# Performance work log

Hardware: AMD Instinct MI355X
Metric: run time of the kernel (lower is better)

The kernel has to match this reference:

```python
import jax, jax.numpy as jnp
import numpy as np

B, S, D, H = 4, 1024, 1024, 16
HD = D // H
MAX_DIST, WIN, MAX_SPAN = 512, 256, 512
TEMP_SCALE = 0.01
EPS = 1e-5


def _ln(x, g, b):
    m = x.mean(-1, keepdims=True)
    v = ((x - m) ** 2).mean(-1, keepdims=True)
    return (x - m) * jax.lax.rsqrt(v + EPS) * g + b


def _heads(t):
    b, s, _ = t.shape
    return t.reshape(b, s, H, HD).transpose(0, 2, 1, 3)


def _merge(t):
    b, _, s, _ = t.shape
    return t.transpose(0, 2, 1, 3).reshape(b, s, D)


def _global_attn(x, Wq, bq, Wk, Wv, bv, Wo, bo):
    # MultiheadC with mask tensor passed -> is_causal=True SDPA (default 1/sqrt(HD) scale)
    q = _heads(x @ Wq.T + bq)
    k = _heads(x @ Wk.T)
    v = _heads(x @ Wv.T + bv)
    s = jnp.einsum('bhqd,bhkd->bhqk', q, k) / float(np.sqrt(HD))
    n = x.shape[1]
    causal = jnp.tril(jnp.ones((n, n), bool))
    s = jnp.where(causal, s, jnp.finfo(s.dtype).min)
    w = jax.nn.softmax(s, axis=-1)
    return _merge(jnp.einsum('bhqk,bhkd->bhqd', w, v)) @ Wo.T + bo


def _span_attn(q, k, v, temp):
    # AdaptiveSpan core: softmax(QK^T / temperature * head_dim**-0.25) V
    scale = HD ** -0.25
    qh, kh, vh = _heads(q), _heads(k), _heads(v)
    w = jax.nn.softmax(jnp.einsum('bhqd,bhkd->bhqk', qh, kh) / temp * scale, axis=-1)
    return _merge(jnp.einsum('bhqk,bhkd->bhqd', w, vh))


def _slide_win(local, span_mean, win, span_len, local_max):
    bx, sx, dx = local.shape
    temp = 1.0 + TEMP_SCALE * (1.0 - span_mean)  # sharpen=True branch
    outs = []
    for st in range(0, sx, win):  # static unrolled loop over windows (ragged slices)
        en = min(st + win, sx)
        wlen = en - st
        ks = max(0, st - span_len + win)
        ke = min(st + span_len, sx)
        klen = ke - ks
        eff = min(int(wlen * span_mean), wlen, klen, local_max)
        if eff <= 0:
            outs.append(jnp.zeros((bx, wlen, dx), local.dtype))
            continue
        o = _span_attn(local[:, st:st + eff], local[:, ks:ks + eff], local[:, ks:ks + eff], temp)
        if eff < wlen:
            o = jnp.concatenate([o, jnp.zeros((bx, wlen - eff, dx), local.dtype)], axis=1)
        outs.append(o)
    return jnp.concatenate(outs, axis=1)


def setup_inputs() -> dict:
    key = jax.random.key(0)
    ks = jax.random.split(key, 8)
    qkv_std = 1.0 / float(np.sqrt(HD))
    return {
        'x': jax.random.normal(ks[0], (B, S, D), jnp.float32),
        'ln_a_g': jnp.ones((D,), jnp.float32),
        'ln_a_b': jnp.zeros((D,), jnp.float32),
        'ln_b_g': jnp.ones((D,), jnp.float32),
        'ln_b_b': jnp.zeros((D,), jnp.float32),
        'Wq': jax.random.normal(ks[1], (D, D), jnp.float32) * qkv_std,
        'bq': jnp.zeros((D,), jnp.float32),
        'Wk': jax.random.normal(ks[2], (D, D), jnp.float32) * qkv_std,
        'Wv': jax.random.normal(ks[3], (D, D), jnp.float32) * qkv_std,
        'bv': jnp.zeros((D,), jnp.float32),
        'Wo': jax.random.normal(ks[4], (D, D), jnp.float32) * 0.02,
        'bo': jnp.zeros((D,), jnp.float32),
        'Wp': jax.random.normal(ks[5], (1, D), jnp.float32) * float(np.sqrt(2.0 / (D + 1))),
        'bp': jnp.zeros((1,), jnp.float32),
        'Wproj': jax.random.normal(ks[6], (D, 2 * D), jnp.float32) * 0.02,
        'bproj': jnp.zeros((D,), jnp.float32),
    }


def reference(x, ln_a_g, ln_a_b, ln_b_g, ln_b_b, Wq, bq, Wk, Wv, bv, Wo, bo, Wp, bp, Wproj, bproj):
    local = _ln(x, ln_a_g, ln_a_b)
    globe = _ln(x, ln_b_g, ln_b_b)
    globe_out = _global_attn(globe, Wq, bq, Wk, Wv, bv, Wo, bo)
    # Predictor: sigmoid(Linear(mean over seq))
    base_scale = jax.nn.sigmoid(globe_out.mean(axis=1) @ Wp.T + bp)  # [B, 1]
    span_scale = jnp.clip(base_scale, 0.0, 1.0)  # RL refine factor fixed at 1.0 (deterministic)
    span_mean = float(jnp.mean(span_scale))  # mirrors torch .item() host sync
    win = max(1, int(WIN * span_mean))
    span_len = max(1, int(MAX_SPAN * span_mean))
    local_max = min(MAX_DIST, span_len, win)
    local_out = _slide_win(local, span_mean, win, span_len, local_max)
    combined = jnp.concatenate([local_out, globe_out], axis=-1)
    return combined @ Wproj.T + bproj
```

## Files before the change

kernel.cpp:

```cpp
#include <hip/hip_runtime.h>
#include <math.h>

#define B_ 4
#define S_ 1024
#define D_ 1024
#define H_ 16
#define HD_ 64
#define BSD_ (B_*S_*D_)

using short8 = __attribute__((ext_vector_type(8))) short;
using f32x4  = __attribute__((ext_vector_type(4))) float;

#define MFMA16(a,b,c) __builtin_amdgcn_mfma_f32_16x16x32_bf16((a),(b),(c),0,0,0)

__device__ __forceinline__ ushort f2bf(float f) {
  uint u = __float_as_uint(f);
  return (ushort)((u + 0x7fffu + ((u >> 16) & 1u)) >> 16);
}
__device__ __forceinline__ float bf2f(ushort h) {
  return __uint_as_float(((uint)h) << 16);
}
__device__ __forceinline__ void split8(const float* p, short8* hi, short8* lo) {
  #pragma unroll
  for (int j = 0; j < 8; j++) {
    ushort h = f2bf(p[j]);
    (*hi)[j] = (short)h;
    (*lo)[j] = (short)f2bf(p[j] - bf2f(h));
  }
}
__device__ __forceinline__ void async_load16(const ushort* g, ushort* l) {
  __builtin_amdgcn_global_load_lds(
      (const __attribute__((address_space(1))) unsigned int*)g,
      (__attribute__((address_space(3))) unsigned int*)l, 16, 0, 0);
}

__device__ __forceinline__ float block_reduce_sum_256(float v, float* sbuf) {
  #pragma unroll
  for (int off = 32; off > 0; off >>= 1) v += __shfl_xor(v, off, 64);
  int lane = threadIdx.x & 63, wid = threadIdx.x >> 6;
  __syncthreads();
  if (lane == 0) sbuf[wid] = v;
  __syncthreads();
  return sbuf[0] + sbuf[1] + sbuf[2] + sbuf[3];
}

__device__ __forceinline__ void split4_store(const float4 a, ushort* orow, int c, int stride) {
  ushort4 hi, lo;
  hi.x = f2bf(a.x); hi.y = f2bf(a.y); hi.z = f2bf(a.z); hi.w = f2bf(a.w);
  lo.x = f2bf(a.x - bf2f(hi.x)); lo.y = f2bf(a.y - bf2f(hi.y));
  lo.z = f2bf(a.z - bf2f(hi.z)); lo.w = f2bf(a.w - bf2f(hi.w));
  *(ushort4*)(orow + c)          = hi;
  *(ushort4*)(orow + stride + c) = lo;
}

__global__ __launch_bounds__(256) void prep_kernel(
    const float* __restrict__ x,
    const float* __restrict__ ln_a_g, const float* __restrict__ ln_a_b,
    const float* __restrict__ ln_b_g, const float* __restrict__ ln_b_b,
    const float* __restrict__ Wq, const float* __restrict__ Wk,
    const float* __restrict__ Wv, const float* __restrict__ bq,
    const float* __restrict__ bv, const float* __restrict__ Wo,
    const float* __restrict__ Wproj,
    ushort* __restrict__ Acat, ushort* __restrict__ Bqkv,
    float* __restrict__ biascat, float* __restrict__ loc,
    ushort* __restrict__ B3, ushort* __restrict__ Bo) {
  __shared__ float sbuf[4];
  const int bx = blockIdx.x;
  const int t = threadIdx.x;
  if (bx < 4096) {
    const int row = bx;
    const int c = t*4;
    const float* xr = x + (size_t)row * D_;
    float4 v = *(const float4*)(xr + c);
    float s = v.x + v.y + v.z + v.w;
    const float mean = block_reduce_sum_256(s, sbuf) * (1.0f/D_);
    float4 dv = make_float4(v.x-mean, v.y-mean, v.z-mean, v.w-mean);
    float sq = dv.x*dv.x + dv.y*dv.y + dv.z*dv.z + dv.w*dv.w;
    const float var = block_reduce_sum_256(sq, sbuf) * (1.0f/D_);
    const float r = rsqrtf(var + 1e-5f);
    float4 gg = *(const float4*)(ln_b_g + c);
    float4 bb = *(const float4*)(ln_b_b + c);
    float4 n;
    n.x = dv.x*r*gg.x + bb.x; n.y = dv.y*r*gg.y + bb.y;
    n.z = dv.z*r*gg.z + bb.z; n.w = dv.w*r*gg.w + bb.w;
    split4_store(n, Acat + (size_t)row*2048, c, 1024);
  } else if (bx < 7168) {
    const int idx = (bx - 4096)*256 + t;
    const int n = idx >> 8;
    const int col4 = (idx & 255) << 2;
    const float* src = (n < 1024) ? (Wq + (size_t)n*1024)
                     : (n < 2048) ? (Wk + (size_t)(n-1024)*1024)
                                  : (Wv + (size_t)(n-2048)*1024);
    const float4 a = *(const float4*)(src + col4);
    split4_store(a, Bqkv + (size_t)n*2048, col4, 1024);
    if (idx < 3072)
      biascat[idx] = (idx < 1024) ? bq[idx] : (idx < 2048) ? 0.f : bv[idx-2048];
  } else if (bx < 11264) {
    const int row = bx - 7168;
    const float* xr = x + (size_t)row * D_;
    float v[4]; float s = 0.f;
    #pragma unroll
    for (int i = 0; i < 4; i++) { v[i] = xr[t + 256*i]; s += v[i]; }
    const float mean = block_reduce_sum_256(s, sbuf) * (1.0f/D_);
    float sq = 0.f;
    #pragma unroll
    for (int i = 0; i < 4; i++) { float d = v[i]-mean; sq += d*d; }
    const float var = block_reduce_sum_256(sq, sbuf) * (1.0f/D_);
    const float r = rsqrtf(var + 1e-5f);
    float* orow = loc + (size_t)row * D_;
    #pragma unroll
    for (int i = 0; i < 4; i++) {
      int c = t + 256*i;
      orow[c] = (v[i]-mean)*r*ln_a_g[c] + ln_a_b[c];
    }
  } else if (bx < 13312) {
    const int idx = (bx - 11264)*256 + t;
    const int row = idx >> 9;
    const int col4 = (idx & 511) << 2;
    const float4 a = *(const float4*)(Wproj + (size_t)row*2048 + col4);
    ushort4 hi;
    hi.x = f2bf(a.x); hi.y = f2bf(a.y); hi.z = f2bf(a.z); hi.w = f2bf(a.w);
    *(ushort4*)(B3 + (size_t)row*2048 + col4) = hi;
  } else {
    const int idx = (bx - 13312)*256 + t;
    const int n = idx >> 8;
    const int col4 = (idx & 255) << 2;
    const float4 a = *(const float4*)(Wo + (size_t)n*1024 + col4);
    split4_store(a, Bo + (size_t)n*2048, col4, 1024);
  }
}

__global__ __launch_bounds__(256) void mfma_gemm_qkv(
    const ushort* __restrict__ A, const ushort* __restrict__ Bw,
    const float* __restrict__ bias,
    ushort* __restrict__ Qsp, ushort* __restrict__ Ksp,
    ushort* __restrict__ Vth, ushort* __restrict__ Vtl, int Kh) {
  __shared__ __align__(16) ushort smem[17408];
  ushort* Ash = smem;
  ushort* Asl = smem + 4096;
  ushort* Bsh = smem + 8192;
  ushort* Bsl = smem + 12288;
  const int lda = 2*Kh;
  const int tid = threadIdx.x;
  const int bm = blockIdx.y * 128, bn = blockIdx.x * 128;
  const int wave = tid >> 6, lane = tid & 63;
  const int wm = wave >> 1, wn = wave & 1;
  const int lm = lane & 15, q = lane >> 4;
  const int lrow = lane >> 2;
  const int sw = (((lane & 3) ^ ((lane >> 3) & 3)) << 3);

  f32x4 acc[4][4];
  #pragma unroll
  for (int i = 0; i < 4; i++)
    #pragma unroll
    for (int j = 0; j < 4; j++)
      acc[i][j] = (f32x4){0.f,0.f,0.f,0.f};

  const ushort* Agh = A  + (size_t)(bm + wave*32 + lrow)*lda + sw;
  const ushort* Agl = Agh + Kh;
  const ushort* Bgh = Bw + (size_t)(bn + wave*32 + lrow)*lda + sw;
  const ushort* Bgl = Bgh + Kh;
  const size_t r16a = (size_t)16*lda;
  ushort* AhD0 = &Ash[(wave*32)*32];      ushort* AhD1 = &Ash[(wave*32+16)*32];
  ushort* AlD0 = &Asl[(wave*32)*32];      ushort* AlD1 = &Asl[(wave*32+16)*32];
  ushort* BhD0 = &Bsh[(wave*32)*32];      ushort* BhD1 = &Bsh[(wave*32+16)*32];
  ushort* BlD0 = &Bsl[(wave*32)*32];      ushort* BlD1 = &Bsl[(wave*32+16)*32];
  const int rsw  = ((q ^ ((lm >> 1) & 3)) << 3);
  const int aoff = (wm*64 + lm)*32 + rsw;
  const int boff = (wn*64 + lm)*32 + rsw;

  for (int k0 = 0; k0 < Kh; k0 += 32) {
    __syncthreads();
    async_load16(Agh + k0, AhD0);
    async_load16(Agh + r16a + k0, AhD1);
    async_load16(Agl + k0, AlD0);
    async_load16(Agl + r16a + k0, AlD1);
    async_load16(Bgh + k0, BhD0);
    async_load16(Bgh + r16a + k0, BhD1);
    async_load16(Bgl + k0, BlD0);
    async_load16(Bgl + r16a + k0, BlD1);
    __syncthreads();
    short8 ah[4], al[4], bh[4], bl[4];
    #pragma unroll
    for (int mt = 0; mt < 4; mt++) {
      ah[mt] = *(const short8*)&Ash[aoff + mt*512];
      al[mt] = *(const short8*)&Asl[aoff + mt*512];
    }
    #pragma unroll
    for (int nt = 0; nt < 4; nt++) {
      bh[nt] = *(const short8*)&Bsh[boff + nt*512];
      bl[nt] = *(const short8*)&Bsl[boff + nt*512];
    }
    #pragma unroll
    for (int mt = 0; mt < 4; mt++)
      #pragma unroll
      for (int nt = 0; nt < 4; nt++) {
        f32x4 a = acc[mt][nt];
        a = MFMA16(ah[mt], bh[nt], a);
        a = MFMA16(al[mt], bh[nt], a);
        a = MFMA16(ah[mt], bl[nt], a);
        acc[mt][nt] = a;
      }
  }

  const int b = bm >> 10, s0 = bm & 1023;
  if (blockIdx.x < 16) {
    ushort* dst = (blockIdx.x < 8) ? Qsp : Ksp;
    const int h = ((bn + wn*64) >> 6) & 15;
    #pragma unroll
    for (int mt = 0; mt < 4; mt++) {
      #pragma unroll
      for (int nt = 0; nt < 4; nt++) {
        const int n = bn + wn*64 + nt*16 + lm;
        const int d = nt*16 + lm;
        const float bb = bias[n];
        #pragma unroll
        for (int reg = 0; reg < 4; reg++) {
          const int s = s0 + wm*64 + mt*16 + q*4 + reg;
          const float val = acc[mt][nt][reg] + bb;
          const ushort hi = f2bf(val);
          const ushort lo = f2bf(val - bf2f(hi));
          ushort* rp = dst + ((size_t)((b*16 + h)*1024 + s))*128;
          rp[d] = hi; rp[64 + d] = lo;
        }
      }
    }
  } else {
    ushort* Th = smem;
    ushort* Tl = smem + 8704;
    #pragma unroll
    for (int c = 0; c < 2; c++) {
      __syncthreads();
      if (wn == c) {
        #pragma unroll
        for (int mt = 0; mt < 4; mt++)
          #pragma unroll
          for (int nt = 0; nt < 4; nt++) {
            const int nl = nt*16 + lm;
            const float bb = bias[bn + c*64 + nl];
            #pragma unroll
            for (int reg = 0; reg < 4; reg++) {
              const int sl = wm*64 + mt*16 + q*4 + reg;
              const float val = acc[mt][nt][reg] + bb;
              const ushort hi = f2bf(val);
              const ushort lo = f2bf(val - bf2f(hi));
              Th[nl*136 + sl] = hi;
              Tl[nl*136 + sl] = lo;
            }
          }
      }
      __syncthreads();
      const int nl = tid >> 2, s32 = (tid & 3)*32;
      const int h = ((bn - 2048 + c*64) >> 6) & 15;
      const size_t drow = ((size_t)((b*16 + h)*64 + nl))*1024 + s0 + s32;
      #pragma unroll
      for (int j = 0; j < 4; j++) {
        *(short8*)(Vth + drow + j*8) = *(const short8*)&Th[nl*136 + s32 + j*8];
        *(short8*)(Vtl + drow + j*8) = *(const short8*)&Tl[nl*136 + s32 + j*8];
      }
    }
  }
}

__global__ __launch_bounds__(256) void mfma_gemm2(
    const ushort* __restrict__ A, const ushort* __restrict__ Bw,
    const float* __restrict__ bias, float* __restrict__ C,
    int Kh, int ldc, ushort* __restrict__ aux) {
  __shared__ __align__(16) ushort Ash[64*32];
  __shared__ __align__(16) ushort Asl[64*32];
  __shared__ __align__(16) ushort Bsh[128*32];
  __shared__ __align__(16) ushort Bsl[128*32];
  const int lda = 2*Kh;
  const int tid = threadIdx.x;
  const int bm = blockIdx.y * 64, bn = blockIdx.x * 128;
  const int wave = tid >> 6, lane = tid & 63;
  const int lm = lane & 15, q = lane >> 4;
  const int lrow = lane >> 2;
  const int sw = (((lane & 3) ^ ((lane >> 3) & 3)) << 3);

  f32x4 acc[4][2];
  #pragma unroll
  for (int i = 0; i < 4; i++)
    #pragma unroll
    for (int j = 0; j < 2; j++)
      acc[i][j] = (f32x4){0.f,0.f,0.f,0.f};

  const ushort* gsrc[6];
  ushort* ldst[6];
  #pragma unroll
  for (int i = 0; i < 6; i++) {
    const int s = wave*6 + i;
    const ushort* gp; ushort* lp;
    if (s < 4)       { gp = A  + (size_t)(bm + s*16 + lrow)*lda + sw;           lp = &Ash[(s*16)*32]; }
    else if (s < 8)  { gp = A  + (size_t)(bm + (s-4)*16 + lrow)*lda + Kh + sw;  lp = &Asl[((s-4)*16)*32]; }
    else if (s < 16) { gp = Bw + (size_t)(bn + (s-8)*16 + lrow)*lda + sw;       lp = &Bsh[((s-8)*16)*32]; }
    else             { gp = Bw + (size_t)(bn + (s-16)*16 + lrow)*lda + Kh + sw; lp = &Bsl[((s-16)*16)*32]; }
    gsrc[i] = gp; ldst[i] = lp;
  }
  const int rsw = ((q ^ ((lm >> 1) & 3)) << 3);
  const int aoff = lm*32 + rsw;
  const int boff = (wave*32 + lm)*32 + rsw;

  for (int k0 = 0; k0 < Kh; k0 += 32) {
    __syncthreads();
    #pragma unroll
    for (int i = 0; i < 6; i++) async_load16(gsrc[i] + k0, ldst[i]);
    __syncthreads();
    short8 ah[4], al[4], bh[2], bl[2];
    #pragma unroll
    for (int mt = 0; mt < 4; mt++) {
      ah[mt] = *(const short8*)&Ash[aoff + mt*512];
      al[mt] = *(const short8*)&Asl[aoff + mt*512];
    }
    #pragma unroll
    for (int nt = 0; nt < 2; nt++) {
      bh[nt] = *(const short8*)&Bsh[boff + nt*512];
      bl[nt] = *(const short8*)&Bsl[boff + nt*512];
    }
    #pragma unroll
    for (int mt = 0; mt < 4; mt++)
      #pragma unroll
      for (int nt = 0; nt < 2; nt++) {
        f32x4 a = acc[mt][nt];
        a = MFMA16(ah[mt], bh[nt], a);
        a = MFMA16(al[mt], bh[nt], a);
        a = MFMA16(ah[mt], bl[nt], a);
        acc[mt][nt] = a;
      }
  }

  #pragma unroll
  for (int mt = 0; mt < 4; mt++) {
    #pragma unroll
    for (int nt = 0; nt < 2; nt++) {
      const int n = bn + wave*32 + nt*16 + lm;
      const float bb = bias ? bias[n] : 0.f;
      #pragma unroll
      for (int reg = 0; reg < 4; reg++) {
        const int m = bm + mt*16 + q*4 + reg;
        const float val = acc[mt][nt][reg] + bb;
        C[(size_t)m*ldc + n] = val;
        if (aux) aux[(size_t)m*2048 + 1024 + n] = f2bf(val);
      }
    }
  }
}

__global__ __launch_bounds__(256) void mfma_gemm(
    const ushort* __restrict__ A, const ushort* __restrict__ Bw,
    const float* __restrict__ bias, float* __restrict__ C,
    int K, int ldc) {
  __shared__ __align__(16) ushort As[64*32];
  __shared__ __align__(16) ushort Bs[128*32];
  const int tid = threadIdx.x;
  const int bm = blockIdx.y * 64, bn = blockIdx.x * 128;
  const int wave = tid >> 6, lane = tid & 63;
  const int lm = lane & 15, q = lane >> 4;
  const int lrow = lane >> 2;
  const int sw = (((lane & 3) ^ ((lane >> 3) & 3)) << 3);

  f32x4 acc[4][2];
  #pragma unroll
  for (int i = 0; i < 4; i++)
    #pragma unroll
    for (int j = 0; j < 2; j++)
      acc[i][j] = (f32x4){0.f,0.f,0.f,0.f};

  const ushort* gsrc[3];
  ushort* ldst[3];
  #pragma unroll
  for (int i = 0; i < 3; i++) {
    const int s = wave*3 + i;
    const ushort* gp; ushort* lp;
    if (s < 4) { gp = A  + (size_t)(bm + s*16 + lrow)*K + sw;     lp = &As[(s*16)*32]; }
    else       { gp = Bw + (size_t)(bn + (s-4)*16 + lrow)*K + sw; lp = &Bs[((s-4)*16)*32]; }
    gsrc[i] = gp; ldst[i] = lp;
  }
  const int rsw = ((q ^ ((lm >> 1) & 3)) << 3);
  const int aoff = lm*32 + rsw;
  const int boff = (wave*32 + lm)*32 + rsw;

  for (int k0 = 0; k0 < K; k0 += 32) {
    __syncthreads();
    #pragma unroll
    for (int i = 0; i < 3; i++) async_load16(gsrc[i] + k0, ldst[i]);
    __syncthreads();
    short8 af[4], bf[2];
    #pragma unroll
    for (int mt = 0; mt < 4; mt++) af[mt] = *(const short8*)&As[aoff + mt*512];
    #pragma unroll
    for (int nt = 0; nt < 2; nt++) bf[nt] = *(const short8*)&Bs[boff + nt*512];
    #pragma unroll
    for (int mt = 0; mt < 4; mt++)
      #pragma unroll
      for (int nt = 0; nt < 2; nt++)
        acc[mt][nt] = MFMA16(af[mt], bf[nt], acc[mt][nt]);
  }

  #pragma unroll
  for (int mt = 0; mt < 4; mt++) {
    #pragma unroll
    for (int nt = 0; nt < 2; nt++) {
      const int n = bn + wave*32 + nt*16 + lm;
      const float bb = bias ? bias[n] : 0.f;
      #pragma unroll
      for (int reg = 0; reg < 4; reg++) {
        const int m = bm + mt*16 + q*4 + reg;
        C[(size_t)m*ldc + n] = acc[mt][nt][reg] + bb;
      }
    }
  }
}

__device__ __forceinline__ void attn_unit(
    int qt, int kt, int w, int lm, int q,
    const short8 qh[2], const short8 ql[2],
    const ushort* Kc, const ushort* Vc, float* Pf,
    f32x4 of[4], float mst[4], float lst[4]) {
  f32x4 sS[4];
  #pragma unroll
  for (int nt = 0; nt < 4; nt++) {
    const ushort* kr = &Kc[(nt*16 + lm)*136 + q*8];
    const short8 kh0 = *(const short8*)(kr);
    const short8 kh1 = *(const short8*)(kr + 32);
    const short8 kl0 = *(const short8*)(kr + 64);
    const short8 kl1 = *(const short8*)(kr + 96);
    f32x4 a = (f32x4){0.f,0.f,0.f,0.f};
    a = MFMA16(qh[0], kh0, a);
    a = MFMA16(ql[0], kh0, a);
    a = MFMA16(qh[0], kl0, a);
    a = MFMA16(qh[1], kh1, a);
    a = MFMA16(ql[1], kh1, a);
    a = MFMA16(qh[1], kl1, a);
    sS[nt] = a;
  }
  const int ktbase = kt*64;
  const int qrow0 = qt*64 + w*16 + q*4;
  #pragma unroll
  for (int rm = 0; rm < 4; rm++) {
    const int qrow = qrow0 + rm;
    float v[4];
    #pragma unroll
    for (int nt = 0; nt < 4; nt++) {
      const int kcol = ktbase + nt*16 + lm;
      const float x = sS[nt][rm]*0.125f;
      v[nt] = (kcol <= qrow) ? x : -INFINITY;
    }
    float tm = fmaxf(fmaxf(v[0],v[1]), fmaxf(v[2],v[3]));
    #pragma unroll
    for (int off = 1; off < 16; off <<= 1) tm = fmaxf(tm, __shfl_xor(tm, off, 64));
    const float nm = fmaxf(mst[rm], tm);
    const float alpha = __expf(mst[rm] - nm);
    float ps = 0.f;
    #pragma unroll
    for (int nt = 0; nt < 4; nt++) {
      float p = __expf(v[nt] - nm);
      sS[nt][rm] = p;
      ps += p;
    }
    #pragma unroll
    for (int off = 1; off < 16; off <<= 1) ps += __shfl_xor(ps, off, 64);
    lst[rm] = lst[rm]*alpha + ps;
    mst[rm] = nm;
    #pragma unroll
    for (int nt = 0; nt < 4; nt++) of[nt][rm] *= alpha;
  }
  #pragma unroll
  for (int rm = 0; rm < 4; rm++)
    #pragma unroll
    for (int nt = 0; nt < 4; nt++)
      Pf[(w*16 + q*4 + rm)*66 + nt*16 + lm] = sS[nt][rm];
  short8 ph[2], pl[2];
  {
    const float* prow = &Pf[(w*16 + lm)*66];
    float pv[16];
    *(float4*)&pv[0]  = *(const float4*)(prow + q*8);
    *(float4*)&pv[4]  = *(const float4*)(prow + q*8 + 4);
    *(float4*)&pv[8]  = *(const float4*)(prow + 32 + q*8);
    *(float4*)&pv[12] = *(const float4*)(prow + 32 + q*8 + 4);
    split8(&pv[0], &ph[0], &pl[0]);
    split8(&pv[8], &ph[1], &pl[1]);
  }
  #pragma unroll
  for (int nt = 0; nt < 4; nt++) {
    const ushort* vr = &Vc[(nt*16 + lm)*136 + q*8];
    const short8 vh0 = *(const short8*)(vr);
    const short8 vh1 = *(const short8*)(vr + 32);
    const short8 vl0 = *(const short8*)(vr + 64);
    const short8 vl1 = *(const short8*)(vr + 96);
    f32x4 a = of[nt];
    a = MFMA16(ph[0], vh0, a);
    a = MFMA16(pl[0], vh0, a);
    a = MFMA16(ph[0], vl0, a);
    a = MFMA16(ph[1], vh1, a);
    a = MFMA16(pl[1], vh1, a);
    a = MFMA16(ph[1], vl1, a);
    of[nt] = a;
  }
}

__global__ __launch_bounds__(256) void gattn_mfma(
    const ushort* __restrict__ Qsp, const ushort* __restrict__ Ksp,
    const ushort* __restrict__ Vth, const ushort* __restrict__ Vtl,
    ushort* __restrict__ Aout) {
  __shared__ __align__(16) ushort Kc[64*136];
  __shared__ __align__(16) ushort Vc[64*136];
  __shared__ __align__(16) float  Pf[64*66];
  const int bh = blockIdx.y;
  const int b = bh >> 4, h = bh & 15;
  const int tid = threadIdx.x;
  const int w = tid >> 6, lane = tid & 63;
  const int lm = lane & 15, q = lane >> 4;
  const ushort* Qb_ = Qsp + (size_t)bh * (1024*128);
  const ushort* Kb_ = Ksp + (size_t)bh * (1024*128);
  const ushort* Vhb = Vth + (size_t)bh * (64*1024);
  const ushort* Vlb = Vtl + (size_t)bh * (64*1024);
  const int qtA = 15 - blockIdx.x;
  const int qtB = blockIdx.x;

  short8 qhA[2], qlA[2], qhB[2], qlB[2];
  {
    const ushort* qr = Qb_ + (size_t)(qtA*64 + w*16 + lm)*128 + q*8;
    qhA[0] = *(const short8*)(qr);
    qhA[1] = *(const short8*)(qr + 32);
    qlA[0] = *(const short8*)(qr + 64);
    qlA[1] = *(const short8*)(qr + 96);
    const ushort* qr2 = Qb_ + (size_t)(qtB*64 + w*16 + lm)*128 + q*8;
    qhB[0] = *(const short8*)(qr2);
    qhB[1] = *(const short8*)(qr2 + 32);
    qlB[0] = *(const short8*)(qr2 + 64);
    qlB[1] = *(const short8*)(qr2 + 96);
  }
  f32x4 ofA[4], ofB[4];
  float mstA[4], lstA[4], mstB[4], lstB[4];
  #pragma unroll
  for (int nt = 0; nt < 4; nt++) {
    ofA[nt] = (f32x4){0.f,0.f,0.f,0.f};
    ofB[nt] = (f32x4){0.f,0.f,0.f,0.f};
  }
  #pragma unroll
  for (int rm = 0; rm < 4; rm++) {
    mstA[rm] = -INFINITY; lstA[rm] = 0.f;
    mstB[rm] = -INFINITY; lstB[rm] = 0.f;
  }

  for (int kt = 0; kt <= qtA; ++kt) {
    __syncthreads();
    #pragma unroll
    for (int i = 0; i < 4; i++) {
      const int slot = i*256 + tid;
      const int row = slot >> 4, c8 = slot & 15;
      *(float4*)&Kc[row*136 + c8*8] =
          *(const float4*)(Kb_ + (size_t)(kt*64 + row)*128 + c8*8);
      const ushort* vsrc = ((c8 < 8) ? Vhb : Vlb) + (size_t)row*1024 + kt*64 + (c8&7)*8;
      *(float4*)&Vc[row*136 + c8*8] = *(const float4*)vsrc;
    }
    __syncthreads();
    attn_unit(qtA, kt, w, lm, q, qhA, qlA, Kc, Vc, Pf, ofA, mstA, lstA);
    if (kt <= qtB)
      attn_unit(qtB, kt, w, lm, q, qhB, qlB, Kc, Vc, Pf, ofB, mstB, lstB);
  }

  #pragma unroll
  for (int rm = 0; rm < 4; rm++) {
    const float invA = 1.0f / lstA[rm];
    const int sA = qtA*64 + w*16 + q*4 + rm;
    ushort* arow = Aout + ((size_t)(b*1024 + sA))*2048 + h*64;
    #pragma unroll
    for (int nt = 0; nt < 4; nt++) {
      const float val = ofA[nt][rm] * invA;
      const ushort hi = f2bf(val);
      arow[nt*16 + lm] = hi;
      arow[1024 + nt*16 + lm] = f2bf(val - bf2f(hi));
    }
    const float invB = 1.0f / lstB[rm];
    const int sB = qtB*64 + w*16 + q*4 + rm;
    ushort* brow = Aout + ((size_t)(b*1024 + sB))*2048 + h*64;
    #pragma unroll
    for (int nt = 0; nt < 4; nt++) {
      const float val = ofB[nt][rm] * invB;
      const ushort hi = f2bf(val);
      brow[nt*16 + lm] = hi;
      brow[1024 + nt*16 + lm] = f2bf(val - bf2f(hi));
    }
  }
}

__global__ __launch_bounds__(256) void seqmean1_kernel(const float* __restrict__ g,
                                                       float* __restrict__ part) {
  const int d = blockIdx.x*256 + threadIdx.x;
  const int sc = blockIdx.y;
  const int b = blockIdx.z;
  const float* p = g + ((size_t)b*S_ + sc*128)*D_ + d;
  float s = 0.f;
  #pragma unroll 4
  for (int i = 0; i < 128; i++) s += p[(size_t)i*D_];
  part[((size_t)(b*8 + sc))*D_ + d] = s;
}
__global__ __launch_bounds__(256) void seqmean2_kernel(const float* __restrict__ part,
                                                       float* __restrict__ mbd) {
  const int d = blockIdx.x*256 + threadIdx.x;
  const int b = blockIdx.y;
  float s = 0.f;
  #pragma unroll
  for (int i = 0; i < 8; i++) s += part[((size_t)(b*8 + i))*D_ + d];
  mbd[b*D_ + d] = s * (1.0f/S_);
}

__global__ __launch_bounds__(256) void predictor_kernel(
    const float* __restrict__ mbd, const float* __restrict__ Wp,
    const float* __restrict__ bp, float* __restrict__ fpar, int* __restrict__ ipar) {
  __shared__ float sbuf[4];
  __shared__ float sdots[4];
  const int tid = threadIdx.x;
  for (int b = 0; b < 4; b++) {
    float psum = 0.f;
    for (int d = tid; d < D_; d += 256) psum += mbd[b*D_ + d]*Wp[d];
    float tot = block_reduce_sum_256(psum, sbuf);
    if (tid == 0) sdots[b] = tot;
  }
  __syncthreads();
  if (tid == 0) {
    float smv = 0.f;
    for (int b = 0; b < 4; b++) {
      float z = sdots[b] + bp[0];
      smv += 1.0f/(1.0f + expf(-z));
    }
    smv *= 0.25f;
    int win = max(1, (int)(256.0f*smv));
    int span_len = max(1, (int)(512.0f*smv));
    int local_max = min(512, min(span_len, win));
    float temp = 1.0f + 0.01f*(1.0f - smv);
    int n_win = (S_ + win - 1)/win;
    fpar[0] = smv; fpar[1] = temp;
    ipar[0] = win; ipar[1] = span_len; ipar[2] = local_max; ipar[3] = n_win;
  }
}

#define LDP 68
__global__ __launch_bounds__(256) void lattn_kernel(
    const float* __restrict__ Lc, ushort* __restrict__ Out,
    const int* __restrict__ ip, const float* __restrict__ fpp) {
  __shared__ __align__(16) float Qs[HD_][LDP];
  __shared__ __align__(16) float KPs[64][LDP];
  __shared__ __align__(16) float Vs[64][LDP];
  const int n_win = ip[3];
  const int win = ip[0], span_len = ip[1], local_max = ip[2];
  const float sm = fpp[0], temp = fpp[1];
  const int bh = blockIdx.y;
  const int b = bh >> 4, h = bh & 15;
  const int tid = threadIdx.x;
  const int tx = tid & 15, ty = tid >> 4;
  const float sc = 0.35355339059327373f / temp;
  for (int w = blockIdx.x; w < n_win; w += gridDim.x) {
    const int st = w * win;
    const int en = min(st + win, S_); const int wlen = en - st;
    const int ks = max(0, st - span_len + win);
    const int ke = min(st + span_len, S_); const int klen = ke - ks;
    int eff = (int)((double)wlen * (double)sm);
    eff = min(min(eff, wlen), min(klen, local_max));
    if (eff > 0) {
      const int nt = (eff + 63) >> 6;
      for (int qt = 0; qt < nt; ++qt) {
        const int qn = min(64, eff - qt*64);
        __syncthreads();
        #pragma unroll
        for (int c = 0; c < 4; c++) {
          int f = tid + c*256;
          int r = f >> 4;
          int dc = (f & 15) << 2;
          float4 q4 = make_float4(0.f,0.f,0.f,0.f);
          if (r < qn) q4 = *(const float4*)(Lc + ((size_t)(b*S_ + st + qt*64 + r)) * D_ + h*HD_ + dc);
          Qs[dc+0][r]=q4.x; Qs[dc+1][r]=q4.y; Qs[dc+2][r]=q4.z; Qs[dc+3][r]=q4.w;
        }
        float o[4][4] = {{0.f,0.f,0.f,0.f},{0.f,0.f,0.f,0.f},{0.f,0.f,0.f,0.f},{0.f,0.f,0.f,0.f}};
        float mrow[4], lrow[4];
        #pragma unroll
        for (int i=0;i<4;i++){ mrow[i] = -INFINITY; lrow[i] = 0.f; }
        for (int kt = 0; kt < nt; ++kt) {
          const int kn = min(64, eff - kt*64);
          __syncthreads();
          #pragma unroll
          for (int c = 0; c < 4; c++) {
            int f = tid + c*256;
            int r = f >> 4;
            int dc = (f & 15) << 2;
            float4 k4 = make_float4(0.f,0.f,0.f,0.f);
            if (r < kn) k4 = *(const float4*)(Lc + ((size_t)(b*S_ + ks + kt*64 + r)) * D_ + h*HD_ + dc);
            KPs[dc+0][r]=k4.x; KPs[dc+1][r]=k4.y; KPs[dc+2][r]=k4.z; KPs[dc+3][r]=k4.w;
            *(float4*)&Vs[r][dc] = k4;
          }
          __syncthreads();
          float s[4][4] = {{0.f,0.f,0.f,0.f},{0.f,0.f,0.f,0.f},{0.f,0.f,0.f,0.f},{0.f,0.f,0.f,0.f}};
          #pragma unroll 8
          for (int d = 0; d < HD_; ++d) {
            const float4 a  = *(const float4*)&Qs[d][ty*4];
            const float4 bb = *(const float4*)&KPs[d][tx*4];
            const float av[4]={a.x,a.y,a.z,a.w};
            const float bv[4]={bb.x,bb.y,bb.z,bb.w};
            #pragma unroll
            for (int i=0;i<4;i++)
              #pragma unroll
              for (int j=0;j<4;j++)
                s[i][j] += av[i]*bv[j];
          }
          #pragma unroll
          for (int i=0;i<4;i++) {
            #pragma unroll
            for (int j=0;j<4;j++) {
              float lg = s[i][j]*sc;
              if (kt*64 + tx*4 + j >= eff) lg = -INFINITY;
              s[i][j] = lg;
            }
          }
          #pragma unroll
          for (int i=0;i<4;i++) {
            float tm = fmaxf(fmaxf(s[i][0],s[i][1]), fmaxf(s[i][2],s[i][3]));
            #pragma unroll
            for (int off=1; off<16; off<<=1) tm = fmaxf(tm, __shfl_xor(tm, off, 64));
            const float nm = fmaxf(mrow[i], tm);
            const float alpha = __expf(mrow[i]-nm);
            float ps = 0.f;
            #pragma unroll
            for (int j=0;j<4;j++){ float p = __expf(s[i][j]-nm); s[i][j]=p; ps += p; }
            #pragma unroll
            for (int off=1; off<16; off<<=1) ps += __shfl_xor(ps, off, 64);
            lrow[i] = lrow[i]*alpha + ps;
            mrow[i] = nm;
            #pragma unroll
            for (int j=0;j<4;j++) o[i][j] *= alpha;
          }
          __syncthreads();
          #pragma unroll
          for (int i=0;i<4;i++)
            #pragma unroll
            for (int j=0;j<4;j++)
              KPs[tx*4+j][ty*4+i] = s[i][j];
          __syncthreads();
          #pragma unroll 8
          for (int kk = 0; kk < 64; ++kk) {
            const float4 a  = *(const float4*)&KPs[kk][ty*4];
            const float4 bb = *(const float4*)&Vs[kk][tx*4];
            const float av[4]={a.x,a.y,a.z,a.w};
            const float bv[4]={bb.x,bb.y,bb.z,bb.w};
            #pragma unroll
            for (int i=0;i<4;i++)
              #pragma unroll
              for (int j=0;j<4;j++)
                o[i][j] += av[i]*bv[j];
          }
        }
        #pragma unroll
        for (int i=0;i<4;i++){
          const int r = ty*4 + i;
          if (r < qn) {
            const float inv = 1.0f / lrow[i];
            ushort4 ov;
            ov.x = f2bf(o[i][0]*inv); ov.y = f2bf(o[i][1]*inv);
            ov.z = f2bf(o[i][2]*inv); ov.w = f2bf(o[i][3]*inv);
            *(ushort4*)(Out + ((size_t)(b*S_ + st + qt*64 + r)) * 2048 + h*HD_ + tx*4) = ov;
          }
        }
      }
    }
    const ushort4 z = {0,0,0,0};
    for (int r = max(eff, 0) + ty; r < wlen; r += 16)
      *(ushort4*)(Out + ((size_t)(b*S_ + st + r)) * 2048 + h*HD_ + tx*4) = z;
  }
}

extern "C" void kernel_launch(void* const* d_in, const int* in_sizes, int n_in,
                              void* d_out, int out_size, void* d_ws, size_t ws_size,
                              hipStream_t stream) {
  const float* x      = (const float*)d_in[0];
  const float* ln_a_g = (const float*)d_in[1];
  const float* ln_a_b = (const float*)d_in[2];
  const float* ln_b_g = (const float*)d_in[3];
  const float* ln_b_b = (const float*)d_in[4];
  const float* Wq     = (const float*)d_in[5];
  const float* bq     = (const float*)d_in[6];
  const float* Wk     = (const float*)d_in[7];
  const float* Wv     = (const float*)d_in[8];
  const float* bv     = (const float*)d_in[9];
  const float* Wo     = (const float*)d_in[10];
  const float* bo     = (const float*)d_in[11];
  const float* Wp     = (const float*)d_in[12];
  const float* bp     = (const float*)d_in[13];
  const float* Wproj  = (const float*)d_in[14];
  const float* bproj  = (const float*)d_in[15];
  float* out = (float*)d_out;
  float* ws  = (float*)d_ws;
  ushort* wsu = (ushort*)d_ws;

  ushort* Qsp = wsu;
  ushort* Ksp = wsu + 8388608;
  ushort* Vth = wsu + 16777216;
  ushort* Vtl = wsu + 20971520;
  ushort* B3  = (ushort*)(ws + 12582912);
  float* glo  = ws + 16777216;
  float* loc  = ws + 20971520;
  float* biascat = ws + 25165824;
  float* mbd  = biascat + 4096;
  float* fpar = mbd + 4096;
  int*   ipar = (int*)(fpar + 8);
  ushort* Acat  = (ushort*)(ws + 25182208);
  ushort* Bqkv  = Acat + 12582912;
  ushort* Bo    = Bqkv + 9437184;
  float*  part = (float*)Acat;
  ushort* A3  = wsu;

  const dim3 blk(256);

  prep_kernel<<<dim3(14336), blk, 0, stream>>>(
      x, ln_a_g, ln_a_b, ln_b_g, ln_b_b, Wq, Wk, Wv, bq, bv, Wo, Wproj,
      Acat, Bqkv, biascat, loc, B3, Bo);
  mfma_gemm_qkv<<<dim3(24, 32), blk, 0, stream>>>(Acat, Bqkv, biascat,
                                                  Qsp, Ksp, Vth, Vtl, 1024);
  gattn_mfma<<<dim3(8, 64), blk, 0, stream>>>(Qsp, Ksp, Vth, Vtl, Acat);
  mfma_gemm2<<<dim3(8, 64), blk, 0, stream>>>(Acat, Bo, bo, glo, 1024, 1024, A3);
  seqmean1_kernel<<<dim3(4, 8, B_), blk, 0, stream>>>(glo, part);
  seqmean2_kernel<<<dim3(4, B_), blk, 0, stream>>>(part, mbd);
  predictor_kernel<<<dim3(1), blk, 0, stream>>>(mbd, Wp, bp, fpar, ipar);
  lattn_kernel<<<dim3(64, B_*H_), blk, 0, stream>>>(loc, A3, ipar, fpar);
  mfma_gemm<<<dim3(8, 64), blk, 0, stream>>>(A3, B3, bproj, out, 2048, 1024);
}
```

Baseline: 447.1 us.

## Add 256x256 eight-wave QKV GEMM with double-buffered async LDS pipeline

Replaces the 128x128 four-wave QKV projection GEMM with a 256x256-tile, 512-thread kernel. It uses 128KB of dynamic LDS double buffering, async global-to-LDS loads interleaved with MFMA phases, explicit vmcnt waits and barriers, setprio around compute, and a grid swizzle across 192 blocks. The aim is more operand reuse and better overlap of loads with split-bf16 MFMA work. In exchange it brings heavy register pressure, a grid of only 192 blocks (tail and occupancy risk), and a fallback path if the large LDS attribute fails.

```diff
diff --git a/kernel.cpp b/kernel.cpp
--- a/kernel.cpp
+++ b/kernel.cpp
@@ -130,6 +130,179 @@
   }
 }
 
+#define BARRIER() asm volatile("s_barrier" ::: "memory")
+#define VMW4 asm volatile("s_waitcnt vmcnt(4)" ::: "memory")
+#define VMW0 asm volatile("s_waitcnt vmcnt(0)" ::: "memory")
+
+#define STAGE_A(half, k0, SBs) do { \
+  _Pragma("unroll") \
+  for (int i_ = 0; i_ < 2; ++i_) { \
+    const int cid_ = wave*2 + i_; \
+    const int hilo_ = cid_ >> 3; const int seg_ = cid_ & 7; \
+    const int row0_ = (seg_>>2)*128 + (seg_&3)*16 + (half)*64; \
+    async_load16(A + ((size_t)(bm + row0_ + lrow) << 11) + (hilo_ << 10) + (k0) + sw, \
+                 (SBs) + hilo_*8192 + row0_*32); \
+  } } while (0)
+
+#define STAGE_B(half, k0, SBs) do { \
+  _Pragma("unroll") \
+  for (int i_ = 0; i_ < 2; ++i_) { \
+    const int cid_ = wave*2 + i_; \
+    const int hilo_ = cid_ >> 3; const int seg_ = cid_ & 7; \
+    const int row0_ = (seg_>>1)*64 + (seg_&1)*16 + (half)*32; \
+    async_load16(Bw + ((size_t)(bn + row0_ + lrow) << 11) + (hilo_ << 10) + (k0) + sw, \
+                 (SBs) + 16384 + hilo_*8192 + row0_*32); \
+  } } while (0)
+
+#define PH(mh, nh, SBc, STG, WT) do { \
+  short8 ah_[4], al_[4], bh_[2], bl_[2]; \
+  _Pragma("unroll") \
+  for (int m4_ = 0; m4_ < 4; ++m4_) { \
+    const int ro_ = (wm*128 + (mh)*64 + m4_*16 + lm)*32 + rsw; \
+    ah_[m4_] = *(const short8*)&(SBc)[ro_]; \
+    al_[m4_] = *(const short8*)&(SBc)[8192 + ro_]; } \
+  _Pragma("unroll") \
+  for (int n2_ = 0; n2_ < 2; ++n2_) { \
+    const int ro_ = (wn*64 + (nh)*32 + n2_*16 + lm)*32 + rsw; \
+    bh_[n2_] = *(const short8*)&(SBc)[16384 + ro_]; \
+    bl_[n2_] = *(const short8*)&(SBc)[24576 + ro_]; } \
+  STG; \
+  WT; \
+  BARRIER(); \
+  __builtin_amdgcn_s_setprio(1); \
+  _Pragma("unroll") \
+  for (int m4_ = 0; m4_ < 4; ++m4_) \
+    _Pragma("unroll") \
+    for (int n2_ = 0; n2_ < 2; ++n2_) { \
+      f32x4 t_ = acc[(mh)*4+m4_][(nh)*2+n2_]; \
+      t_ = MFMA16(ah_[m4_], bh_[n2_], t_); \
+      t_ = MFMA16(al_[m4_], bh_[n2_], t_); \
+      t_ = MFMA16(ah_[m4_], bl_[n2_], t_); \
+      acc[(mh)*4+m4_][(nh)*2+n2_] = t_; } \
+  __builtin_amdgcn_s_setprio(0); \
+  BARRIER(); \
+} while (0)
+
+#define GROUP(t, SBc, SBs) do { \
+  const int k0n_ = (((t) + 1) & 31) * 32; \
+  PH(0, 0, (SBc), STAGE_A(0, k0n_, (SBs)), VMW4); \
+  PH(0, 1, (SBc), STAGE_B(0, k0n_, (SBs)), VMW4); \
+  PH(1, 0, (SBc), STAGE_B(1, k0n_, (SBs)), ((void)0)); \
+  PH(1, 1, (SBc), STAGE_A(1, k0n_, (SBs)), VMW4); \
+} while (0)
+
+__global__ __launch_bounds__(512, 2) void qkv8_kernel(
+    const ushort* __restrict__ A, const ushort* __restrict__ Bw,
+    const float* __restrict__ bias,
+    ushort* __restrict__ Qsp, ushort* __restrict__ Ksp,
+    ushort* __restrict__ Vth, ushort* __restrict__ Vtl) {
+  extern __shared__ __align__(16) ushort smem[];
+  const int tid = threadIdx.x;
+  const int wave = tid >> 6, lane = tid & 63;
+  const int wm = wave >> 2, wn = wave & 3;
+  const int lm = lane & 15, q = lane >> 4;
+  const int lrow = lane >> 2;
+  const int sw = (((lane & 3) ^ ((lane >> 3) & 3)) << 3);
+  const int rsw = ((q ^ ((lm >> 1) & 3)) << 3);
+  const int bid = blockIdx.x;
+  const int swz = (bid & 7) * 24 + (bid >> 3);
+  const int bm = (swz / 12) * 256;
+  const int bn = (swz % 12) * 256;
+
+  f32x4 acc[8][4];
+  #pragma unroll
+  for (int i = 0; i < 8; ++i)
+    #pragma unroll
+    for (int j = 0; j < 4; ++j) acc[i][j] = (f32x4){0.f,0.f,0.f,0.f};
+
+  STAGE_A(0, 0, smem); STAGE_B(0, 0, smem); STAGE_B(1, 0, smem); STAGE_A(1, 0, smem);
+  VMW0; BARRIER();
+
+  #pragma unroll 1
+  for (int g = 0; g < 32; g += 2) {
+    GROUP(g,     smem,         smem + 32768);
+    GROUP(g + 1, smem + 32768, smem);
+  }
+  VMW0;
+  __syncthreads();
+
+  const int b = bm >> 10, s0 = bm & 1023;
+  if (bn < 2048) {
+    ushort* dst = (bn < 1024) ? Qsp : Ksp;
+    #pragma unroll
+    for (int m = 0; m < 8; ++m) {
+      const int s = s0 + wm*128 + m*16 + q*4;
+      #pragma unroll
+      for (int n = 0; n < 4; ++n) {
+        const int ncol = bn + wn*64 + n*16 + lm;
+        const int h = (ncol >> 6) & 15;
+        const int d = ncol & 63;
+        const float bb = bias[ncol];
+        #pragma unroll
+        for (int reg = 0; reg < 4; ++reg) {
+          const float val = acc[m][n][reg] + bb;
+          const ushort hi = f2bf(val);
+          ushort* rp = dst + ((size_t)((b*16 + h)*1024 + (s + reg)))*128;
+          rp[d] = hi; rp[64 + d] = f2bf(val - bf2f(hi));
+        }
+      }
+    }
+  } else {
+    const int h = ((bn - 2048) >> 6) + wn;
+    ushort* Tbuf = smem + wn * 8704;
+    const size_t vrow0 = (size_t)((b*16 + h) * 64);
+    #pragma unroll 1
+    for (int r = 0; r < 2; ++r) {
+      __syncthreads();
+      if (wm == r) {
+        #pragma unroll
+        for (int m = 0; m < 8; ++m)
+          #pragma unroll
+          for (int n = 0; n < 4; ++n) {
+            const int d = n*16 + lm;
+            const float bb = bias[bn + wn*64 + d];
+            #pragma unroll
+            for (int reg = 0; reg < 4; ++reg)
+              Tbuf[d*136 + m*16 + q*4 + reg] = f2bf(acc[m][n][reg] + bb);
+          }
+        #pragma unroll
+        for (int dd = 0; dd < 4; ++dd) {
+          const int d = (lane >> 2) + dd*16;
+          #pragma unroll
+          for (int j = 0; j < 4; ++j) {
+            const int sc = (lane & 3)*32 + j*8;
+            *(short8*)(Vth + (vrow0 + d)*1024 + s0 + wm*128 + sc) =
+                *(const short8*)&Tbuf[d*136 + sc];
+          }
+        }
+        #pragma unroll
+        for (int m = 0; m < 8; ++m)
+          #pragma unroll
+          for (int n = 0; n < 4; ++n) {
+            const int d = n*16 + lm;
+            const float bb = bias[bn + wn*64 + d];
+            #pragma unroll
+            for (int reg = 0; reg < 4; ++reg) {
+              const float val = acc[m][n][reg] + bb;
+              const ushort hi = f2bf(val);
+              Tbuf[d*136 + m*16 + q*4 + reg] = f2bf(val - bf2f(hi));
+            }
+          }
+        #pragma unroll
+        for (int dd = 0; dd < 4; ++dd) {
+          const int d = (lane >> 2) + dd*16;
+          #pragma unroll
+          for (int j = 0; j < 4; ++j) {
+            const int sc = (lane & 3)*32 + j*8;
+            *(short8*)(Vtl + (vrow0 + d)*1024 + s0 + wm*128 + sc) =
+                *(const short8*)&Tbuf[d*136 + sc];
+          }
+        }
+      }
+    }
+  }
+}
+
 __global__ __launch_bounds__(256) void mfma_gemm_qkv(
     const ushort* __restrict__ A, const ushort* __restrict__ Bw,
     const float* __restrict__ bias,
@@ -206,12 +379,12 @@
   const int b = bm >> 10, s0 = bm & 1023;
   if (blockIdx.x < 16) {
     ushort* dst = (blockIdx.x < 8) ? Qsp : Ksp;
-    const int h = ((bn + wn*64) >> 6) & 15;
     #pragma unroll
     for (int mt = 0; mt < 4; mt++) {
       #pragma unroll
       for (int nt = 0; nt < 4; nt++) {
         const int n = bn + wn*64 + nt*16 + lm;
+        const int h = (n >> 6) & 15;
         const int d = nt*16 + lm;
         const float bb = bias[n];
         #pragma unroll
@@ -811,11 +984,23 @@
 
   const dim3 blk(256);
 
+  static int qkv_path = -1;
+  if (qkv_path < 0) {
+    hipError_t e = hipFuncSetAttribute(
+        reinterpret_cast<const void*>(qkv8_kernel),
+        hipFuncAttributeMaxDynamicSharedMemorySize, 131072);
+    qkv_path = (e == hipSuccess) ? 1 : 0;
+  }
+
   prep_kernel<<<dim3(14336), blk, 0, stream>>>(
       x, ln_a_g, ln_a_b, ln_b_g, ln_b_b, Wq, Wk, Wv, bq, bv, Wo, Wproj,
       Acat, Bqkv, biascat, loc, B3, Bo);
-  mfma_gemm_qkv<<<dim3(24, 32), blk, 0, stream>>>(Acat, Bqkv, biascat,
-                                                  Qsp, Ksp, Vth, Vtl, 1024);
+  if (qkv_path)
+    qkv8_kernel<<<dim3(192), dim3(512), 131072, stream>>>(
+        Acat, Bqkv, biascat, Qsp, Ksp, Vth, Vtl);
+  else
+    mfma_gemm_qkv<<<dim3(24, 32), blk, 0, stream>>>(Acat, Bqkv, biascat,
+                                                    Qsp, Ksp, Vth, Vtl, 1024);
   gattn_mfma<<<dim3(8, 64), blk, 0, stream>>>(Qsp, Ksp, Vth, Vtl, Acat);
   mfma_gemm2<<<dim3(8, 64), blk, 0, stream>>>(Acat, Bo, bo, glo, 1024, 1024, A3);
   seqmean1_kernel<<<dim3(4, 8, B_), blk, 0, stream>>>(glo, part);
```

Result: no change. 442.9 us (-0.9%).

## Add double-buffered async-load QKV GEMM kernel with phased MFMA scheduling

Applied to the files above, without the earlier changes.

Adds a new QKV projection GEMM kernel that double-buffers LDS tiles (64KB dynamic shared memory) using async global-to-LDS loads. It splits each K-step into four sub-phases that interleave the loads with MFMA work, using explicit vmcnt waits, barriers and setprio. The aim is to hide global memory latency behind the split-bf16 MFMA compute. The old kernel is kept as a fallback if the shared-memory attribute cannot be set, at the cost of more barriers and lower occupancy from the larger LDS footprint.

```diff
diff --git a/kernel.cpp b/kernel.cpp
--- a/kernel.cpp
+++ b/kernel.cpp
@@ -130,6 +130,169 @@
   }
 }
 
+#define BARRIER() asm volatile("s_barrier" ::: "memory")
+#define VMW(n)  asm volatile("s_waitcnt vmcnt(" #n ")" ::: "memory")
+
+#define STAGE4(k0, SBs) do { \
+  _Pragma("unroll") \
+  for (int i_ = 0; i_ < 2; ++i_) { \
+    const int cid_ = wave*2 + i_, hl_ = cid_>>2, rs_ = cid_&3; \
+    const int r0_ = (rs_>>1)*64 + (rs_&1)*16; \
+    async_load16(A  + ((size_t)(bm + r0_ + lrow) << 11) + (hl_ << 10) + (k0) + sw, \
+                 (SBs) + hl_*4096 + r0_*32); \
+  } \
+  _Pragma("unroll") \
+  for (int i_ = 0; i_ < 2; ++i_) { \
+    const int cid_ = wave*2 + i_, hl_ = cid_>>2, rs_ = cid_&3; \
+    const int r0_ = (rs_>>1)*64 + (rs_&1)*16; \
+    async_load16(Bw + ((size_t)(bn + r0_ + lrow) << 11) + (hl_ << 10) + (k0) + sw, \
+                 (SBs) + 8192 + hl_*4096 + r0_*32); \
+  } \
+  _Pragma("unroll") \
+  for (int i_ = 0; i_ < 2; ++i_) { \
+    const int cid_ = wave*2 + i_, hl_ = cid_>>2, rs_ = cid_&3; \
+    const int r1_ = (rs_>>1)*64 + (rs_&1)*16 + 32; \
+    async_load16(Bw + ((size_t)(bn + r1_ + lrow) << 11) + (hl_ << 10) + (k0) + sw, \
+                 (SBs) + 8192 + hl_*4096 + r1_*32); \
+  } \
+  _Pragma("unroll") \
+  for (int i_ = 0; i_ < 2; ++i_) { \
+    const int cid_ = wave*2 + i_, hl_ = cid_>>2, rs_ = cid_&3; \
+    const int r1_ = (rs_>>1)*64 + (rs_&1)*16 + 32; \
+    async_load16(A  + ((size_t)(bm + r1_ + lrow) << 11) + (hl_ << 10) + (k0) + sw, \
+                 (SBs) + hl_*4096 + r1_*32); \
+  } \
+} while (0)
+
+#define PH4(mh, nh, SBc, STG, WT) do { \
+  short8 ah_[2], al_[2], bh_[2], bl_[2]; \
+  _Pragma("unroll") \
+  for (int m4_ = 0; m4_ < 2; ++m4_) { \
+    const int ro_ = (wm*64 + (mh)*32 + m4_*16 + lm)*32 + rsw; \
+    ah_[m4_] = *(const short8*)&(SBc)[ro_]; \
+    al_[m4_] = *(const short8*)&(SBc)[4096 + ro_]; } \
+  _Pragma("unroll") \
+  for (int n2_ = 0; n2_ < 2; ++n2_) { \
+    const int ro_ = (wn*64 + (nh)*32 + n2_*16 + lm)*32 + rsw; \
+    bh_[n2_] = *(const short8*)&(SBc)[8192 + ro_]; \
+    bl_[n2_] = *(const short8*)&(SBc)[12288 + ro_]; } \
+  STG; \
+  WT; \
+  BARRIER(); \
+  __builtin_amdgcn_s_setprio(1); \
+  _Pragma("unroll") \
+  for (int m4_ = 0; m4_ < 2; ++m4_) \
+    _Pragma("unroll") \
+    for (int n2_ = 0; n2_ < 2; ++n2_) { \
+      f32x4 t_ = acc[(mh)*2+m4_][(nh)*2+n2_]; \
+      t_ = MFMA16(ah_[m4_], bh_[n2_], t_); \
+      t_ = MFMA16(al_[m4_], bh_[n2_], t_); \
+      t_ = MFMA16(ah_[m4_], bl_[n2_], t_); \
+      acc[(mh)*2+m4_][(nh)*2+n2_] = t_; } \
+  __builtin_amdgcn_s_setprio(0); \
+  BARRIER(); \
+} while (0)
+
+#define GROUP4(g, SBc, SBs) do { \
+  const int k0n_ = (((g) + 1) & 31) * 32; \
+  PH4(0, 0, (SBc), STAGE4(k0n_, (SBs)), VMW(10)); \
+  PH4(0, 1, (SBc), ((void)0), VMW(8)); \
+  PH4(1, 0, (SBc), ((void)0), ((void)0)); \
+  PH4(1, 1, (SBc), ((void)0), VMW(4)); \
+} while (0)
+
+__global__ __launch_bounds__(256, 2) void qkv4_kernel(
+    const ushort* __restrict__ A, const ushort* __restrict__ Bw,
+    const float* __restrict__ bias,
+    ushort* __restrict__ Qsp, ushort* __restrict__ Ksp,
+    ushort* __restrict__ Vth, ushort* __restrict__ Vtl) {
+  extern __shared__ __align__(16) ushort smem[];
+  const int tid = threadIdx.x;
+  const int bm = blockIdx.y * 128, bn = blockIdx.x * 128;
+  const int wave = tid >> 6, lane = tid & 63;
+  const int wm = wave >> 1, wn = wave & 1;
+  const int lm = lane & 15, q = lane >> 4;
+  const int lrow = lane >> 2;
+  const int sw = (((lane & 3) ^ ((lane >> 3) & 3)) << 3);
+  const int rsw = ((q ^ ((lm >> 1) & 3)) << 3);
+
+  f32x4 acc[4][4];
+  #pragma unroll
+  for (int i = 0; i < 4; i++)
+    #pragma unroll
+    for (int j = 0; j < 4; j++)
+      acc[i][j] = (f32x4){0.f,0.f,0.f,0.f};
+
+  STAGE4(0, smem);
+  VMW(4); BARRIER();
+
+  #pragma unroll 1
+  for (int g = 0; g < 32; g += 2) {
+    GROUP4(g,     smem,         smem + 16384);
+    GROUP4(g + 1, smem + 16384, smem);
+  }
+  VMW(0);
+  __syncthreads();
+
+  const int b = bm >> 10, s0 = bm & 1023;
+  if (blockIdx.x < 16) {
+    ushort* dst = (blockIdx.x < 8) ? Qsp : Ksp;
+    #pragma unroll
+    for (int mt = 0; mt < 4; mt++) {
+      #pragma unroll
+      for (int nt = 0; nt < 4; nt++) {
+        const int n = bn + wn*64 + nt*16 + lm;
+        const int h = (n >> 6) & 15;
+        const int d = nt*16 + lm;
+        const float bb = bias[n];
+        #pragma unroll
+        for (int reg = 0; reg < 4; reg++) {
+          const int s = s0 + wm*64 + mt*16 + q*4 + reg;
+          const float val = acc[mt][nt][reg] + bb;
+          const ushort hi = f2bf(val);
+          const ushort lo = f2bf(val - bf2f(hi));
+          ushort* rp = dst + ((size_t)((b*16 + h)*1024 + s))*128;
+          rp[d] = hi; rp[64 + d] = lo;
+        }
+      }
+    }
+  } else {
+    ushort* Th = smem;
+    ushort* Tl = smem + 8704;
+    #pragma unroll
+    for (int c = 0; c < 2; c++) {
+      __syncthreads();
+      if (wn == c) {
+        #pragma unroll
+        for (int mt = 0; mt < 4; mt++)
+          #pragma unroll
+          for (int nt = 0; nt < 4; nt++) {
+            const int nl = nt*16 + lm;
+            const float bb = bias[bn + c*64 + nl];
+            #pragma unroll
+            for (int reg = 0; reg < 4; reg++) {
+              const int sl = wm*64 + mt*16 + q*4 + reg;
+              const float val = acc[mt][nt][reg] + bb;
+              const ushort hi = f2bf(val);
+              const ushort lo = f2bf(val - bf2f(hi));
+              Th[nl*136 + sl] = hi;
+              Tl[nl*136 + sl] = lo;
+            }
+          }
+      }
+      __syncthreads();
+      const int nl = tid >> 2, s32 = (tid & 3)*32;
+      const int h = ((bn - 2048 + c*64) >> 6) & 15;
+      const size_t drow = ((size_t)((b*16 + h)*64 + nl))*1024 + s0 + s32;
+      #pragma unroll
+      for (int j = 0; j < 4; j++) {
+        *(short8*)(Vth + drow + j*8) = *(const short8*)&Th[nl*136 + s32 + j*8];
+        *(short8*)(Vtl + drow + j*8) = *(const short8*)&Tl[nl*136 + s32 + j*8];
+      }
+    }
+  }
+}
+
 __global__ __launch_bounds__(256) void mfma_gemm_qkv(
     const ushort* __restrict__ A, const ushort* __restrict__ Bw,
     const float* __restrict__ bias,
@@ -206,12 +369,12 @@
   const int b = bm >> 10, s0 = bm & 1023;
   if (blockIdx.x < 16) {
     ushort* dst = (blockIdx.x < 8) ? Qsp : Ksp;
-    const int h = ((bn + wn*64) >> 6) & 15;
     #pragma unroll
     for (int mt = 0; mt < 4; mt++) {
       #pragma unroll
       for (int nt = 0; nt < 4; nt++) {
         const int n = bn + wn*64 + nt*16 + lm;
+        const int h = (n >> 6) & 15;
         const int d = nt*16 + lm;
         const float bb = bias[n];
         #pragma unroll
@@ -811,11 +974,23 @@
 
   const dim3 blk(256);
 
+  static int qkv_path = -1;
+  if (qkv_path < 0) {
+    hipError_t e = hipFuncSetAttribute(
+        reinterpret_cast<const void*>(qkv4_kernel),
+        hipFuncAttributeMaxDynamicSharedMemorySize, 65536);
+    qkv_path = (e == hipSuccess) ? 1 : 0;
+  }
+
   prep_kernel<<<dim3(14336), blk, 0, stream>>>(
       x, ln_a_g, ln_a_b, ln_b_g, ln_b_b, Wq, Wk, Wv, bq, bv, Wo, Wproj,
       Acat, Bqkv, biascat, loc, B3, Bo);
-  mfma_gemm_qkv<<<dim3(24, 32), blk, 0, stream>>>(Acat, Bqkv, biascat,
-                                                  Qsp, Ksp, Vth, Vtl, 1024);
+  if (qkv_path)
+    qkv4_kernel<<<dim3(24, 32), blk, 65536, stream>>>(
+        Acat, Bqkv, biascat, Qsp, Ksp, Vth, Vtl);
+  else
+    mfma_gemm_qkv<<<dim3(24, 32), blk, 0, stream>>>(Acat, Bqkv, biascat,
+                                                    Qsp, Ksp, Vth, Vtl, 1024);
   gattn_mfma<<<dim3(8, 64), blk, 0, stream>>>(Qsp, Ksp, Vth, Vtl, Acat);
   mfma_gemm2<<<dim3(8, 64), blk, 0, stream>>>(Acat, Bo, bo, glo, 1024, 1024, A3);
   seqmean1_kernel<<<dim3(4, 8, B_), blk, 0, stream>>>(glo, part);
```

Result: no change. 441.5 us (-1.2%).
